# Performance work log

Measured on AMD Instinct MI355X. Metric: run time of the kernel, lower is better.

The kernel has to match this reference:

```python
import jax, jax.numpy as jnp
import numpy as np

# Render constants matching GaussianRenderer(__init__): image size and top-K blend depth.
H, W, K = 128, 128, 10
N_G = 2048  # number of gaussians


def setup_inputs() -> dict:
    key = jax.random.key(0)
    k1, k2, k3, k4 = jax.random.split(key, 4)
    # Means in pixel coordinates so gaussians cover the image.
    gaussian_means = jax.random.uniform(k1, (N_G, 2), dtype=jnp.float32) * jnp.array([W, H], jnp.float32)
    # Rotation angle per gaussian in [0, 2pi).
    gaussian_rotations = jax.random.uniform(k2, (N_G,), dtype=jnp.float32) * (2.0 * np.pi)
    # log std-devs centered at log(3) => ~3px footprint.
    gaussian_log_scales = jax.random.normal(k3, (N_G, 2), dtype=jnp.float32) * 0.3 + np.log(3.0)
    gaussian_colors = jax.random.uniform(k4, (N_G, 3), dtype=jnp.float32)
    return {
        "gaussian_means": gaussian_means,
        "gaussian_rotations": gaussian_rotations,
        "gaussian_log_scales": gaussian_log_scales,
        "gaussian_colors": gaussian_colors,
    }


def reference(gaussian_means, gaussian_rotations, gaussian_log_scales, gaussian_colors):
    """2D Gaussian splatting: per-pixel top-K gaussians by opacity, alpha-composited.

    Covariance per gaussian: Sigma = R(theta) diag(exp(2*log_scales)) R(theta)^T.
    alpha_i(p) = exp(-0.5 * d^T Sigma^{-1} d), d = p - mean_i.
    Per pixel, the K gaussians with largest alpha are blended front-to-back:
        out = sum_i color_i * alpha_i * prod_{j<i} (1 - alpha_j).
    (The torch module's tile binning + max_G_per_tile is a GPU performance
    optimization; the dense evaluation here computes the same per-pixel math.)
    """
    cos_t = jnp.cos(gaussian_rotations)  # [N]
    sin_t = jnp.sin(gaussian_rotations)
    inv_var = jnp.exp(-2.0 * gaussian_log_scales)  # [N,2] = 1/sigma^2 per axis
    ivx, ivy = inv_var[:, 0], inv_var[:, 1]
    # Sigma^{-1} = R diag(1/sx^2, 1/sy^2) R^T  (symmetric 2x2: [[a, b], [b, c]])
    a = cos_t * cos_t * ivx + sin_t * sin_t * ivy  # [N]
    c = sin_t * sin_t * ivx + cos_t * cos_t * ivy
    b = cos_t * sin_t * (ivx - ivy)

    xs = jnp.arange(W, dtype=jnp.float32) + 0.5
    ys = jnp.arange(H, dtype=jnp.float32) + 0.5
    px, py = jnp.meshgrid(xs, ys)  # [H,W] each
    dx = px.reshape(-1, 1) - gaussian_means[:, 0]  # [P, N], P = H*W
    dy = py.reshape(-1, 1) - gaussian_means[:, 1]
    q = a * dx * dx + 2.0 * b * dx * dy + c * dy * dy  # Mahalanobis distance^2 [P,N]
    alpha = jnp.exp(-0.5 * q)  # [P,N] in (0,1]

    top_alpha, top_idx = jax.lax.top_k(alpha, K)  # [P,K], descending alpha
    # Front-to-back transmittance: T_0 = 1, T_i = prod_{j<i} (1 - alpha_j)
    trans = jnp.cumprod(1.0 - top_alpha, axis=1)
    trans = jnp.concatenate([jnp.ones_like(trans[:, :1]), trans[:, :-1]], axis=1)
    weight = top_alpha * trans  # [P,K]
    top_colors = gaussian_colors[top_idx]  # [P,K,3]
    image = jnp.einsum("pk,pkc->pc", weight, top_colors).reshape(H, W, 3)
    return image
```

## Files before the change

### kernel.cpp

```cpp
#include <hip/hip_runtime.h>

#define HH 128
#define WW 128
#define NPX (HH * WW)
#define KK 10
#define PXB 16
#define TPP 16
#define LCAP 352
#define SCAP 176
#define SPAD 177
#define ALPHA_MIN 5e-4f
#define RADIUS_K 3.8990f

__device__ __forceinline__ bool beats(float a, int ai, float b, int bi) {
  return (a > b) || (a == b && ai < bi);
}

__device__ __forceinline__ void insert_tb(float vals[KK], int ids[KK], float v,
                                          int vi) {
#pragma unroll
  for (int k = 0; k < KK; ++k) {
    bool sw = beats(v, vi, vals[k], ids[k]);
    float tv = vals[k];
    int ti = ids[k];
    vals[k] = sw ? v : tv;
    ids[k]  = sw ? vi : ti;
    v  = sw ? tv : v;
    vi = sw ? ti : vi;
  }
}

__global__ __launch_bounds__(256) void splat_kernel(
    const float* __restrict__ means, const float* __restrict__ rots,
    const float* __restrict__ lscales, const float* __restrict__ cols,
    int nG, float* __restrict__ out) {
  __shared__ float4 sA[LCAP];
  __shared__ float  sMy[LCAP];
  __shared__ int    glist[LCAP];
  __shared__ float2 sbuf[PXB][SPAD];
  __shared__ int    scnt[PXB];
  __shared__ int    lcnt;

  int t  = threadIdx.x;
  int pl = t & 15;
  int ts = t >> 4;
  int tile = blockIdx.x;
  int x0 = (tile & 31) << 2;
  int y0 = (tile >> 5) << 2;
  int x = x0 | (pl & 3);
  int y = y0 | (pl >> 2);
  float px = (float)x + 0.5f, py = (float)y + 0.5f;

  if (t == 0) lcnt = 0;
  if (t < PXB) scnt[t] = 0;
  __syncthreads();

  float rx0 = (float)x0 + 0.5f, rx1 = (float)x0 + 3.5f;
  float ry0 = (float)y0 + 0.5f, ry1 = (float)y0 + 3.5f;
  for (int g = t; g < nG; g += 256) {
    float mx = means[2 * g], my = means[2 * g + 1];
    float smax = __expf(fmaxf(lscales[2 * g], lscales[2 * g + 1]));
    float r = RADIUS_K * smax * 1.01f + 0.05f;
    float cx = fminf(fmaxf(mx, rx0), rx1) - mx;
    float cy = fminf(fmaxf(my, ry0), ry1) - my;
    if (cx * cx + cy * cy <= r * r) {
      int idx = atomicAdd(&lcnt, 1);
      if (idx < LCAP) glist[idx] = g;
    }
  }
  __syncthreads();
  int cnt = min(lcnt, LCAP);

  for (int i = t; i < cnt; i += 256) {
    int g = glist[i];
    float th = rots[g];
    float s = __sinf(th), c = __cosf(th);
    float ivx = __expf(-2.0f * lscales[2 * g]);
    float ivy = __expf(-2.0f * lscales[2 * g + 1]);
    float a  = c * c * ivx + s * s * ivy;
    float cc = s * s * ivx + c * c * ivy;
    float b2 = 2.0f * (c * s * (ivx - ivy));
    sA[i]  = make_float4(a, b2, cc, means[2 * g]);
    sMy[i] = means[2 * g + 1];
  }
  __syncthreads();

  for (int i = ts; i < cnt; i += TPP) {
    float4 q0 = sA[i];
    float dx = px - q0.w;
    float dy = py - sMy[i];
    float q = fmaf(dx, fmaf(q0.y, dy, q0.x * dx), q0.z * dy * dy);
    float a = __expf(-0.5f * q);
    if (a >= ALPHA_MIN) {
      int idx = atomicAdd(&scnt[pl], 1);
      if (idx < SCAP) sbuf[pl][idx] = make_float2(a, __int_as_float(glist[i]));
    }
  }
  __syncthreads();

  if (t < 2 * PXB) {
    int p2 = t >> 1, half = t & 1;
    int sc = min(scnt[p2], SCAP);
    float vals[KK];
    int ids[KK];
#pragma unroll
    for (int k = 0; k < KK; ++k) { vals[k] = 0.0f; ids[k] = 0; }
    for (int i = half; i < sc; i += 2) {
      float2 e = sbuf[p2][i];
      float a = e.x;
      int id = __float_as_int(e.y);
      if (beats(a, id, vals[KK - 1], ids[KK - 1])) insert_tb(vals, ids, a, id);
    }
    float ov[KK];
    int oi[KK];
#pragma unroll
    for (int k = 0; k < KK; ++k) {
      ov[k] = __shfl_xor(vals[k], 1);
      oi[k] = __shfl_xor(ids[k], 1);
    }
    if (half == 0) {
#pragma unroll
      for (int k = 0; k < KK; ++k) {
        if (!beats(ov[k], oi[k], vals[KK - 1], ids[KK - 1])) break;
        insert_tb(vals, ids, ov[k], oi[k]);
      }
      int xx = x0 | (p2 & 3);
      int yy = y0 | (p2 >> 2);
      int pp = yy * WW + xx;
      float trans = 1.0f, r = 0.0f, g = 0.0f, b = 0.0f;
#pragma unroll
      for (int k = 0; k < KK; ++k) {
        float a = vals[k];
        float w = a * trans;
        int id = ids[k];
        r += w * cols[3 * id + 0];
        g += w * cols[3 * id + 1];
        b += w * cols[3 * id + 2];
        trans *= (1.0f - a);
      }
      out[3 * pp + 0] = r;
      out[3 * pp + 1] = g;
      out[3 * pp + 2] = b;
    }
  }
}

extern "C" void kernel_launch(void* const* d_in, const int* in_sizes, int n_in,
                              void* d_out, int out_size, void* d_ws, size_t ws_size,
                              hipStream_t stream) {
  const float* means   = (const float*)d_in[0];
  const float* rots    = (const float*)d_in[1];
  const float* lscales = (const float*)d_in[2];
  const float* cols    = (const float*)d_in[3];
  float* out = (float*)d_out;
  int nG = in_sizes[1];

  splat_kernel<<<NPX / PXB, 256, 0, stream>>>(means, rots, lscales, cols, nG, out);
}
```

Before: 84.27 us.

## Fuse gaussian preprocessing into culling and prune candidates with per-pixel top-K threshold

Computes conic parameters directly in the culling loop, which removes a separate pass and one barrier, and loads means and scales as float2. Alpha values for each pixel are held in registers (JMAX=22 slots per thread). Each thread's maximum goes to shared memory, and a per-pixel lower bound is taken as the 10th largest of the 16 thread maxima, which is a valid lower bound on the true 10th-largest alpha. Only candidates at or above that bound are pushed into the selection buffer, which shrinks the serial top-K insertion work. In exchange it adds register pressure and an extra barrier, shrinks SCAP to 128, and silently drops gaussians beyond index ts+21*16 if cnt exceeds 352.

```diff
diff --git a/kernel.cpp b/kernel.cpp
--- a/kernel.cpp
+++ b/kernel.cpp
@@ -7,8 +7,10 @@
 #define PXB 16
 #define TPP 16
 #define LCAP 352
-#define SCAP 176
-#define SPAD 177
+#define JMAX 22
+#define SCAP 128
+#define SPAD 129
+#define SMPAD 17
 #define ALPHA_MIN 5e-4f
 #define RADIUS_K 3.8990f
 
@@ -30,6 +32,16 @@
   }
 }
 
+__device__ __forceinline__ void bubble_vals10(float vals[KK], float v) {
+#pragma unroll
+  for (int k = 0; k < KK; ++k) {
+    float tv = vals[k];
+    bool sw = v > tv;
+    vals[k] = sw ? v : tv;
+    v = sw ? tv : v;
+  }
+}
+
 __global__ __launch_bounds__(256) void splat_kernel(
     const float* __restrict__ means, const float* __restrict__ rots,
     const float* __restrict__ lscales, const float* __restrict__ cols,
@@ -37,6 +49,8 @@
   __shared__ float4 sA[LCAP];
   __shared__ float  sMy[LCAP];
   __shared__ int    glist[LCAP];
+  __shared__ float  smax[PXB * SMPAD];
+  __shared__ float  stau[PXB];
   __shared__ float2 sbuf[PXB][SPAD];
   __shared__ int    scnt[PXB];
   __shared__ int    lcnt;
@@ -55,43 +69,70 @@
   if (t < PXB) scnt[t] = 0;
   __syncthreads();
 
+  const float2* m2 = (const float2*)means;
+  const float2* l2 = (const float2*)lscales;
   float rx0 = (float)x0 + 0.5f, rx1 = (float)x0 + 3.5f;
   float ry0 = (float)y0 + 0.5f, ry1 = (float)y0 + 3.5f;
   for (int g = t; g < nG; g += 256) {
-    float mx = means[2 * g], my = means[2 * g + 1];
-    float smax = __expf(fmaxf(lscales[2 * g], lscales[2 * g + 1]));
-    float r = RADIUS_K * smax * 1.01f + 0.05f;
-    float cx = fminf(fmaxf(mx, rx0), rx1) - mx;
-    float cy = fminf(fmaxf(my, ry0), ry1) - my;
+    float2 mg = m2[g];
+    float2 lg = l2[g];
+    float smx = __expf(fmaxf(lg.x, lg.y));
+    float r = fmaf(RADIUS_K * 1.01f, smx, 0.05f);
+    float cx = fminf(fmaxf(mg.x, rx0), rx1) - mg.x;
+    float cy = fminf(fmaxf(mg.y, ry0), ry1) - mg.y;
     if (cx * cx + cy * cy <= r * r) {
       int idx = atomicAdd(&lcnt, 1);
-      if (idx < LCAP) glist[idx] = g;
+      if (idx < LCAP) {
+        float th = rots[g];
+        float s = __sinf(th), c = __cosf(th);
+        float ivx = __expf(-2.0f * lg.x);
+        float ivy = __expf(-2.0f * lg.y);
+        sA[idx] = make_float4(c * c * ivx + s * s * ivy,
+                              2.0f * (c * s * (ivx - ivy)),
+                              s * s * ivx + c * c * ivy, mg.x);
+        sMy[idx] = mg.y;
+        glist[idx] = g;
+      }
     }
   }
   __syncthreads();
   int cnt = min(lcnt, LCAP);
 
-  for (int i = t; i < cnt; i += 256) {
-    int g = glist[i];
-    float th = rots[g];
-    float s = __sinf(th), c = __cosf(th);
-    float ivx = __expf(-2.0f * lscales[2 * g]);
-    float ivy = __expf(-2.0f * lscales[2 * g + 1]);
-    float a  = c * c * ivx + s * s * ivy;
-    float cc = s * s * ivx + c * c * ivy;
-    float b2 = 2.0f * (c * s * (ivx - ivy));
-    sA[i]  = make_float4(a, b2, cc, means[2 * g]);
-    sMy[i] = means[2 * g + 1];
-  }
-  __syncthreads();
-
-  for (int i = ts; i < cnt; i += TPP) {
-    float4 q0 = sA[i];
-    float dx = px - q0.w;
-    float dy = py - sMy[i];
-    float q = fmaf(dx, fmaf(q0.y, dy, q0.x * dx), q0.z * dy * dy);
-    float a = __expf(-0.5f * q);
-    if (a >= ALPHA_MIN) {
+  float ra[JMAX];
+  float mymax = 0.0f;
+#pragma unroll
+  for (int j = 0; j < JMAX; ++j) {
+    int i = ts + j * TPP;
+    float a = 0.0f;
+    if (i < cnt) {
+      float4 q0 = sA[i];
+      float dx = px - q0.w;
+      float dy = py - sMy[i];
+      float q = fmaf(dx, fmaf(q0.y, dy, q0.x * dx), q0.z * dy * dy);
+      a = __expf(-0.5f * q);
+    }
+    ra[j] = a;
+    mymax = fmaxf(mymax, a);
+  }
+  smax[pl * SMPAD + ts] = mymax;
+  __syncthreads();
+
+  if (t < PXB) {
+    float tv[KK];
+#pragma unroll
+    for (int k = 0; k < KK; ++k) tv[k] = 0.0f;
+#pragma unroll
+    for (int j = 0; j < TPP; ++j) bubble_vals10(tv, smax[t * SMPAD + j]);
+    stau[t] = fmaxf(tv[KK - 1], ALPHA_MIN);
+  }
+  __syncthreads();
+
+  float tau = stau[pl];
+#pragma unroll
+  for (int j = 0; j < JMAX; ++j) {
+    int i = ts + j * TPP;
+    float a = ra[j];
+    if (a >= tau) {
       int idx = atomicAdd(&scnt[pl], 1);
       if (idx < SCAP) sbuf[pl][idx] = make_float2(a, __int_as_float(glist[i]));
     }
```

Result: faster. 76.01 us (-9.8%).
